# Optimization experiments

Hardware: AMD Instinct MI355X
Metric: run time of the kernel (lower is better)

## Reference

```python
import jax, jax.numpy as jnp
import numpy as np

ATOL = 1e-06
RTOL = 1e-06

def setup_inputs() -> dict:
    key = jax.random.key(0)
    ks = jax.random.split(key, 8)
    u = lambda k, shape: jax.random.uniform(k, shape, jnp.float32, -0.05, 0.05)
    return {
        "x": jax.random.normal(ks[0], (4096, 32, 32, 3), jnp.float32),
        "W_lstm": u(ks[1], (3, 16)),      # input kernel, gates [i,f,c,o]
        "U_lstm": u(ks[2], (4, 16)),      # recurrent kernel
        "dw_kernel": u(ks[3], (27, 27, 3, 5)),  # depthwise (kh,kw,in_c,mult)
        "pw_kernel": u(ks[4], (15, 4)),   # pointwise
        "conv_bias": u(ks[5], (4,)),
        "W_td": u(ks[6], (4096, 10)),
        "W_sc": u(ks[7], (4096, 10)),
    }

def _lstm_td(x, W, U):
    # TimeDistributed LSTM: x (B,32,32,3) -> treat axis1 as TD batch, axis2 as time
    B = x.shape[0]
    seq = x.reshape(B * 32, 32, 3)          # (N, T, F)
    xs = jnp.transpose(seq, (1, 0, 2))      # (T, N, F)
    N = seq.shape[0]
    h0 = jnp.zeros((N, 4), x.dtype)
    c0 = jnp.zeros((N, 4), x.dtype)

    def step(carry, xt):
        h, c = carry
        z = xt @ W + h @ U                  # (N, 16)
        zi, zf, zc, zo = jnp.split(z, 4, axis=-1)
        i = jax.nn.elu(zi)                  # recurrent_activation='elu'
        f = jax.nn.elu(zf)
        c = f * c + i * jax.nn.softmax(zc, axis=-1)  # activation='softmax'
        o = jax.nn.elu(zo)
        h = o * jax.nn.softmax(c, axis=-1)
        return (h, c), h

    _, hs = jax.lax.scan(step, (h0, c0), xs)        # (T, N, 4)
    return jnp.transpose(hs, (1, 0, 2)).reshape(B, 32, 32, 4)

def _sep_conv(x, dw_kernel, pw_kernel, conv_bias):
    # depthwise: Keras (kh,kw,C,M) -> lax HWIO grouped (kh,kw,1,C*M), channel-major order
    dw = dw_kernel.reshape(27, 27, 1, 15)
    y = jax.lax.conv_general_dilated(
        x, dw, window_strides=(1, 1), padding='SAME',
        feature_group_count=3,
        dimension_numbers=('NHWC', 'HWIO', 'NHWC'))   # (B,32,32,15)
    y = jnp.einsum('bhwc,cf->bhwf', y, pw_kernel) + conv_bias
    return jax.nn.sigmoid(y)                          # (B,32,32,4)

def reference(x, W_lstm, U_lstm, dw_kernel, pw_kernel, conv_bias, W_td, W_sc):
    B = x.shape[0]
    td = _lstm_td(x, W_lstm, U_lstm).reshape(B, -1) @ W_td   # (B,10)
    sc = _sep_conv(x, dw_kernel, pw_kernel, conv_bias).reshape(B, -1) @ W_sc
    diff = jnp.abs(td - sc)
    tol = ATOL + RTOL * jnp.abs(sc)
    return diff <= tol
```

## Files before the change

kernel.cpp:

```cpp
#include <hip/hip_runtime.h>
#include <math.h>

#define TD_OFF 0
#define WTDR_OFF 40960
#define SC_OFF 81920
#define BG_BYTE_OFF 524288

typedef __bf16 bf16x8 __attribute__((ext_vector_type(8)));
typedef float f32x16 __attribute__((ext_vector_type(16)));

union FragU { bf16x8 v; float4 f; };

__device__ __forceinline__ f32x16 mfma16(bf16x8 a, bf16x8 b, f32x16 c) {
    return __builtin_amdgcn_mfma_f32_32x32x16_bf16(a, b, c, 0, 0, 0);
}

__device__ __forceinline__ float eluf(float v) {
    return v > 0.f ? v : __expf(v) - 1.f;
}

__global__ __launch_bounds__(256) void prep(const float* __restrict__ dw,
                                            const float* __restrict__ pw,
                                            const float* __restrict__ Wtd,
                                            float* __restrict__ Wtdr,
                                            unsigned short* __restrict__ Bg) {
    int gid = blockIdx.x * 256 + threadIdx.x;
    if (gid < 40960) {
        int k = gid & 3;
        int r = gid >> 2;
        int row = r & 31; r >>= 5;
        int j = r % 10;
        int tt = r / 10;
        Wtdr[gid] = Wtd[(size_t)(row * 128 + tt * 4 + k) * 10 + j];
        return;
    }
    int g2 = gid - 40960;
    if (g2 >= 162 * 128) return;
    int n = g2 & 127;
    int s = g2 >> 7;
    int half = s & 1;
    int cd = s >> 1;
    int c = cd / 27, d = cd % 27;
    int w = n >> 2, f = n & 3;
    unsigned short* dsth = Bg + (size_t)s * 4096 + n * 16;
    unsigned short* dstl = dsth + 2048;
#pragma unroll
    for (int k = 0; k < 16; k++) {
        int xi = half * 16 + k;
        int dx = xi - w + 13;
        float v = 0.f;
        if (dx >= 0 && dx < 27) {
#pragma unroll
            for (int m = 0; m < 5; m++)
                v = fmaf(dw[((d * 27 + dx) * 3 + c) * 5 + m],
                         pw[(c * 5 + m) * 4 + f], v);
        }
        __bf16 h = (__bf16)v;
        __bf16 l = (__bf16)(v - (float)h);
        dsth[k] = __builtin_bit_cast(unsigned short, h);
        dstl[k] = __builtin_bit_cast(unsigned short, l);
    }
}

#define A_OFF 0
#define ZOFF 49152
#define SRED_OFF 49168
#define LDS_BYTES 49488

__global__ __launch_bounds__(256, 3) void fused(const float* __restrict__ x,
                                                const float* __restrict__ W,
                                                const float* __restrict__ U,
                                                const float* __restrict__ Wtdr,
                                                const unsigned short* __restrict__ Bg,
                                                const float* __restrict__ Wsc,
                                                const float* __restrict__ bias,
                                                float* __restrict__ td_out,
                                                float* __restrict__ sc_out) {
    __shared__ char LDS[LDS_BYTES] __attribute__((aligned(16)));
    int bx = blockIdx.x;
    int rem = bx % 3;
    int q = bx / 3;
    int t = threadIdx.x;

    if (rem == 2) {
        float rW[48], rU[64];
        const float4* W4 = (const float4*)W;
        const float4* U4 = (const float4*)U;
#pragma unroll
        for (int i = 0; i < 12; i++) {
            float4 qv = W4[i];
            rW[i * 4 + 0] = qv.x; rW[i * 4 + 1] = qv.y;
            rW[i * 4 + 2] = qv.z; rW[i * 4 + 3] = qv.w;
        }
#pragma unroll
        for (int i = 0; i < 16; i++) {
            float4 qv = U4[i];
            rU[i * 4 + 0] = qv.x; rU[i * 4 + 1] = qv.y;
            rU[i * 4 + 2] = qv.z; rU[i * 4 + 3] = qv.w;
        }

        int n = q * 256 + t;
        int row = n & 31;
        const float4* xp4 = (const float4*)(x + (size_t)n * 96);

        float h0 = 0, h1 = 0, h2 = 0, h3 = 0;
        float c0 = 0, c1 = 0, c2 = 0, c3 = 0;
        float acc[10];
#pragma unroll
        for (int j = 0; j < 10; j++) acc[j] = 0.f;

        for (int g = 0; g < 8; g++) {
            float4 q0 = xp4[g * 3 + 0], q1 = xp4[g * 3 + 1], q2 = xp4[g * 3 + 2];
            float xr[12] = {q0.x, q0.y, q0.z, q0.w, q1.x, q1.y,
                            q1.z, q1.w, q2.x, q2.y, q2.z, q2.w};
#pragma unroll
            for (int st = 0; st < 4; st++) {
                int tt = g * 4 + st;
                float x0 = xr[st * 3 + 0], x1 = xr[st * 3 + 1], x2 = xr[st * 3 + 2];
                float z[16];
#pragma unroll
                for (int k = 0; k < 16; k++)
                    z[k] = x0 * rW[k] + x1 * rW[16 + k] + x2 * rW[32 + k]
                         + h0 * rU[k] + h1 * rU[16 + k] + h2 * rU[32 + k] + h3 * rU[48 + k];

                float ig0 = eluf(z[0]),  ig1 = eluf(z[1]),  ig2 = eluf(z[2]),  ig3 = eluf(z[3]);
                float fg0 = eluf(z[4]),  fg1 = eluf(z[5]),  fg2 = eluf(z[6]),  fg3 = eluf(z[7]);
                float og0 = eluf(z[12]), og1 = eluf(z[13]), og2 = eluf(z[14]), og3 = eluf(z[15]);

                float zm = fmaxf(fmaxf(z[8], z[9]), fmaxf(z[10], z[11]));
                float e0 = __expf(z[8] - zm), e1 = __expf(z[9] - zm);
                float e2 = __expf(z[10] - zm), e3 = __expf(z[11] - zm);
                float inv = 1.f / (e0 + e1 + e2 + e3);
                c0 = fg0 * c0 + ig0 * (e0 * inv);
                c1 = fg1 * c1 + ig1 * (e1 * inv);
                c2 = fg2 * c2 + ig2 * (e2 * inv);
                c3 = fg3 * c3 + ig3 * (e3 * inv);

                float cm = fmaxf(fmaxf(c0, c1), fmaxf(c2, c3));
                float p0 = __expf(c0 - cm), p1 = __expf(c1 - cm);
                float p2 = __expf(c2 - cm), p3 = __expf(c3 - cm);
                float pinv = 1.f / (p0 + p1 + p2 + p3);
                h0 = og0 * (p0 * pinv); h1 = og1 * (p1 * pinv);
                h2 = og2 * (p2 * pinv); h3 = og3 * (p3 * pinv);

                const float4* wr4 = (const float4*)(Wtdr + (size_t)tt * 1280) + row;
#pragma unroll
                for (int j = 0; j < 10; j++) {
                    float4 qv = wr4[j * 32];
                    acc[j] += h0 * qv.x + h1 * qv.y + h2 * qv.z + h3 * qv.w;
                }
            }
        }

#pragma unroll
        for (int off = 16; off >= 1; off >>= 1) {
#pragma unroll
            for (int j = 0; j < 10; j++) acc[j] += __shfl_xor(acc[j], off, 64);
        }
        int lane = t & 63;
        if (lane == 0 || lane == 32) {
            int b = n >> 5;
#pragma unroll
            for (int j = 0; j < 10; j++) td_out[b * 10 + j] = acc[j];
        }
        return;
    }

    int ci = q * 2 + rem;
    int l = t & 63;
    int wv = t >> 6;
    int m = l & 31;
    int sub = l >> 5;
    int img0 = (wv >> 1) * 2;
    int ntbase = (wv & 1) * 2;

    const char* bbase = (const char*)Bg + (size_t)ntbase * 1024 + m * 32 + sub * 16;
    FragU bufA[4], bufB[4];
#define LOADB(sv, arr) { const char* p_ = bbase + (size_t)(sv) * 8192;       \
        arr[0].f = *(const float4*)(p_);                         \
        arr[1].f = *(const float4*)(p_ + 4096);                  \
        arr[2].f = *(const float4*)(p_ + 1024);                  \
        arr[3].f = *(const float4*)(p_ + 5120); }

    LOADB(0, bufA);
    LOADB(1, bufB);

    const float4* xb4 = (const float4*)(x + (size_t)ci * 12288);
#pragma unroll
    for (int it = 0; it < 12; it++) {
        int fi = it * 256 + t;
        float4 qv = xb4[fi];
        float vals[4] = {qv.x, qv.y, qv.z, qv.w};
#pragma unroll
        for (int e = 0; e < 4; e++) {
            int pel = fi * 4 + e;
            int im = pel / 3072;
            int p = pel - im * 3072;
            int c = p % 3;
            int hw = p / 3;
            int w = hw & 31;
            int h = hw >> 5;
            int rec = A_OFF + im * 12288
                      + ((c * 8) + (w >> 4) * 2 + ((w >> 3) & 1)) * 512
                      + h * 16 + (w & 7) * 2;
            float v = vals[e];
            __bf16 hb = (__bf16)v;
            __bf16 lb = (__bf16)(v - (float)hb);
            *(__bf16*)(LDS + rec) = hb;
            *(__bf16*)(LDS + rec + 2048) = lb;
        }
    }
    if (t < 4) *(float*)(LDS + ZOFF + t * 4) = 0.f;
    __syncthreads();

    f32x16 acc00 = {0,0,0,0,0,0,0,0,0,0,0,0,0,0,0,0};
    f32x16 acc01 = acc00, acc10 = acc00, acc11 = acc00;

    int c = 0, d = 0, half = 0;

#define CHUNK(USE, SNEXT) {                                                   \
    int rowIdx = m + d - 13;                                                  \
    bool valid = (unsigned)rowIdx < 32u;                                      \
    int a0 = A_OFF + img0 * 12288 + (c * 8 + half * 2 + sub) * 512 + rowIdx * 16; \
    int ah0o = valid ? a0 : ZOFF;                                             \
    int al0o = valid ? (a0 + 2048) : ZOFF;                                    \
    int ah1o = valid ? (a0 + 12288) : ZOFF;                                   \
    int al1o = valid ? (a0 + 14336) : ZOFF;                                   \
    FragU ah0, al0, ah1, al1;                                                 \
    ah0.f = *(const float4*)(LDS + ah0o);                                     \
    al0.f = *(const float4*)(LDS + al0o);                                     \
    ah1.f = *(const float4*)(LDS + ah1o);                                     \
    al1.f = *(const float4*)(LDS + al1o);                                     \
    acc00 = mfma16(ah0.v, USE[0].v, acc00);                                   \
    acc01 = mfma16(ah0.v, USE[2].v, acc01);                                   \
    acc10 = mfma16(ah1.v, USE[0].v, acc10);                                   \
    acc11 = mfma16(ah1.v, USE[2].v, acc11);                                   \
    acc00 = mfma16(ah0.v, USE[1].v, acc00);                                   \
    acc01 = mfma16(ah0.v, USE[3].v, acc01);                                   \
    acc10 = mfma16(ah1.v, USE[1].v, acc10);                                   \
    acc11 = mfma16(ah1.v, USE[3].v, acc11);                                   \
    acc00 = mfma16(al0.v, USE[0].v, acc00);                                   \
    acc01 = mfma16(al0.v, USE[2].v, acc01);                                   \
    acc10 = mfma16(al1.v, USE[0].v, acc10);                                   \
    acc11 = mfma16(al1.v, USE[2].v, acc11);                                   \
    LOADB(SNEXT, USE);                                                        \
    half ^= 1;                                                                \
    if (!half) { d++; if (d == 27) { d = 0; c++; } }                          \
}

    for (int g = 0; g < 81; g++) {
        CHUNK(bufA, 2 * g + 2);
        CHUNK(bufB, 2 * g + 3);
    }

    float b4[4];
#pragma unroll
    for (int i = 0; i < 4; i++) b4[i] = bias[i];

    float part[2][10];
#pragma unroll
    for (int i = 0; i < 2; i++)
#pragma unroll
        for (int j = 0; j < 10; j++) part[i][j] = 0.f;

    f32x16 accs[2][2] = {{acc00, acc01}, {acc10, acc11}};
#pragma unroll
    for (int i2 = 0; i2 < 2; i2++) {
#pragma unroll
        for (int j2 = 0; j2 < 2; j2++) {
            int ncol = (ntbase + j2) * 32 + m;
            int wcol = ncol >> 2;
            int f = ncol & 3;
            f32x16 a = accs[i2][j2];
#pragma unroll
            for (int r = 0; r < 16; r++) {
                int h = (r & 3) + 8 * (r >> 2) + 4 * sub;
                float v = a[r] + b4[f];
                float sg = 1.f / (1.f + expf(-v));
                const float* wr = Wsc + (size_t)((h * 32 + wcol) * 4 + f) * 10;
#pragma unroll
                for (int j = 0; j < 10; j++) part[i2][j] = fmaf(sg, wr[j], part[i2][j]);
            }
        }
    }

#pragma unroll
    for (int off = 32; off >= 1; off >>= 1) {
#pragma unroll
        for (int i2 = 0; i2 < 2; i2++)
#pragma unroll
            for (int j = 0; j < 10; j++) part[i2][j] += __shfl_xor(part[i2][j], off, 64);
    }
    if (l == 0) {
        float* red = (float*)(LDS + SRED_OFF);
#pragma unroll
        for (int i2 = 0; i2 < 2; i2++)
#pragma unroll
            for (int j = 0; j < 10; j++) red[(wv * 2 + i2) * 10 + j] = part[i2][j];
    }
    __syncthreads();
    if (t < 40) {
        int img = t / 10, j = t % 10;
        const float* red = (const float*)(LDS + SRED_OFF);
        int pair = img >> 1, i2 = img & 1;
        float sv = red[((pair * 2) * 2 + i2) * 10 + j]
                 + red[((pair * 2 + 1) * 2 + i2) * 10 + j];
        sc_out[(ci * 4 + img) * 10 + j] = sv;
    }
}

__global__ __launch_bounds__(256) void cmp_k(const float* __restrict__ td,
                                             const float* __restrict__ sc,
                                             float* __restrict__ out) {
    int i = blockIdx.x * 256 + threadIdx.x;
    if (i < 40960) {
        float a = td[i];
        float s = sc[i];
        float tol = 1e-6f + 1e-6f * fabsf(s);
        out[i] = (fabsf(a - s) <= tol) ? 1.0f : 0.0f;
    }
}

extern "C" void kernel_launch(void* const* d_in, const int* in_sizes, int n_in,
                              void* d_out, int out_size, void* d_ws, size_t ws_size,
                              hipStream_t stream) {
    const float* x    = (const float*)d_in[0];
    const float* W    = (const float*)d_in[1];
    const float* U    = (const float*)d_in[2];
    const float* dw   = (const float*)d_in[3];
    const float* pw   = (const float*)d_in[4];
    const float* bias = (const float*)d_in[5];
    const float* Wtd  = (const float*)d_in[6];
    const float* Wsc  = (const float*)d_in[7];

    float* ws     = (float*)d_ws;
    float* td_acc = ws + TD_OFF;
    float* Wtdr   = ws + WTDR_OFF;
    float* sc_acc = ws + SC_OFF;
    unsigned short* Bg = (unsigned short*)((char*)d_ws + BG_BYTE_OFF);

    prep<<<241, 256, 0, stream>>>(dw, pw, Wtd, Wtdr, Bg);
    fused<<<1536, 256, 0, stream>>>(x, W, U, Wtdr, Bg, Wsc, bias, td_acc, sc_acc);
    cmp_k<<<160, 256, 0, stream>>>(td_acc, sc_acc, (float*)d_out);
}
```

Before: 369.3 us.

## Remap conv waves to one N-tile across four images with triple-buffered B loads

Each wave now handles a single 32-column output tile for all four images instead of two tiles for two images. Each wave therefore loads half as much B-fragment data from global memory per chunk, and those loads go through a three-deep rotating buffer. The input staging is rewritten so each thread reads contiguous float4 rows and writes packed 16-byte bf16 hi/lo fragments to LDS instead of scalar 2-byte stores. The epilogue loads each Wsc row once and reuses it for all four images. In exchange, each chunk issues twice as many LDS A-fragment reads, and the larger partial arrays and extra buffer raise register pressure.

```diff
diff --git a/kernel.cpp b/kernel.cpp
--- a/kernel.cpp
+++ b/kernel.cpp
@@ -65,7 +65,7 @@
 #define A_OFF 0
 #define ZOFF 49152
 #define SRED_OFF 49168
-#define LDS_BYTES 49488
+#define LDS_BYTES 49808
 
 __global__ __launch_bounds__(256, 3) void fused(const float* __restrict__ x,
                                                 const float* __restrict__ W,
@@ -171,140 +171,141 @@
     int wv = t >> 6;
     int m = l & 31;
     int sub = l >> 5;
-    int img0 = (wv >> 1) * 2;
-    int ntbase = (wv & 1) * 2;
-
-    const char* bbase = (const char*)Bg + (size_t)ntbase * 1024 + m * 32 + sub * 16;
-    FragU bufA[4], bufB[4];
+
+    const char* bbase = (const char*)Bg + (size_t)wv * 1024 + m * 32 + sub * 16;
+    FragU bufA[2], bufB[2], bufC[2];
 #define LOADB(sv, arr) { const char* p_ = bbase + (size_t)(sv) * 8192;       \
-        arr[0].f = *(const float4*)(p_);                         \
-        arr[1].f = *(const float4*)(p_ + 4096);                  \
-        arr[2].f = *(const float4*)(p_ + 1024);                  \
-        arr[3].f = *(const float4*)(p_ + 5120); }
+        arr[0].f = *(const float4*)(p_);                             \
+        arr[1].f = *(const float4*)(p_ + 4096); }
 
     LOADB(0, bufA);
     LOADB(1, bufB);
-
-    const float4* xb4 = (const float4*)(x + (size_t)ci * 12288);
-#pragma unroll
-    for (int it = 0; it < 12; it++) {
-        int fi = it * 256 + t;
-        float4 qv = xb4[fi];
-        float vals[4] = {qv.x, qv.y, qv.z, qv.w};
-#pragma unroll
-        for (int e = 0; e < 4; e++) {
-            int pel = fi * 4 + e;
-            int im = pel / 3072;
-            int p = pel - im * 3072;
-            int c = p % 3;
-            int hw = p / 3;
-            int w = hw & 31;
-            int h = hw >> 5;
-            int rec = A_OFF + im * 12288
-                      + ((c * 8) + (w >> 4) * 2 + ((w >> 3) & 1)) * 512
-                      + h * 16 + (w & 7) * 2;
-            float v = vals[e];
-            __bf16 hb = (__bf16)v;
-            __bf16 lb = (__bf16)(v - (float)hb);
-            *(__bf16*)(LDS + rec) = hb;
-            *(__bf16*)(LDS + rec + 2048) = lb;
+    LOADB(2, bufC);
+
+    const float* xb = x + (size_t)ci * 12288;
+#pragma unroll
+    for (int rep = 0; rep < 2; rep++) {
+        int u = rep * 256 + t;
+        int im = u >> 7;
+        int woct = (u >> 5) & 3;
+        int h = u & 31;
+        const float4* src = (const float4*)(xb + im * 3072 + h * 96 + woct * 24);
+        float xr[24];
+#pragma unroll
+        for (int i = 0; i < 6; i++) {
+            float4 qv = src[i];
+            xr[i * 4 + 0] = qv.x; xr[i * 4 + 1] = qv.y;
+            xr[i * 4 + 2] = qv.z; xr[i * 4 + 3] = qv.w;
+        }
+#pragma unroll
+        for (int c = 0; c < 3; c++) {
+            FragU hiF, loF;
+#pragma unroll
+            for (int k = 0; k < 8; k++) {
+                float v = xr[k * 3 + c];
+                __bf16 hb = (__bf16)v;
+                hiF.v[k] = hb;
+                loF.v[k] = (__bf16)(v - (float)hb);
+            }
+            int rec = A_OFF + im * 12288 + (c * 8 + woct) * 512 + h * 16;
+            *(float4*)(LDS + rec) = hiF.f;
+            *(float4*)(LDS + rec + 2048) = loF.f;
         }
     }
     if (t < 4) *(float*)(LDS + ZOFF + t * 4) = 0.f;
     __syncthreads();
 
-    f32x16 acc00 = {0,0,0,0,0,0,0,0,0,0,0,0,0,0,0,0};
-    f32x16 acc01 = acc00, acc10 = acc00, acc11 = acc00;
+    f32x16 acc0 = {0,0,0,0,0,0,0,0,0,0,0,0,0,0,0,0};
+    f32x16 acc1 = acc0, acc2 = acc0, acc3 = acc0;
 
     int c = 0, d = 0, half = 0;
 
 #define CHUNK(USE, SNEXT) {                                                   \
     int rowIdx = m + d - 13;                                                  \
     bool valid = (unsigned)rowIdx < 32u;                                      \
-    int a0 = A_OFF + img0 * 12288 + (c * 8 + half * 2 + sub) * 512 + rowIdx * 16; \
-    int ah0o = valid ? a0 : ZOFF;                                             \
-    int al0o = valid ? (a0 + 2048) : ZOFF;                                    \
-    int ah1o = valid ? (a0 + 12288) : ZOFF;                                   \
-    int al1o = valid ? (a0 + 14336) : ZOFF;                                   \
-    FragU ah0, al0, ah1, al1;                                                 \
-    ah0.f = *(const float4*)(LDS + ah0o);                                     \
-    al0.f = *(const float4*)(LDS + al0o);                                     \
-    ah1.f = *(const float4*)(LDS + ah1o);                                     \
-    al1.f = *(const float4*)(LDS + al1o);                                     \
-    acc00 = mfma16(ah0.v, USE[0].v, acc00);                                   \
-    acc01 = mfma16(ah0.v, USE[2].v, acc01);                                   \
-    acc10 = mfma16(ah1.v, USE[0].v, acc10);                                   \
-    acc11 = mfma16(ah1.v, USE[2].v, acc11);                                   \
-    acc00 = mfma16(ah0.v, USE[1].v, acc00);                                   \
-    acc01 = mfma16(ah0.v, USE[3].v, acc01);                                   \
-    acc10 = mfma16(ah1.v, USE[1].v, acc10);                                   \
-    acc11 = mfma16(ah1.v, USE[3].v, acc11);                                   \
-    acc00 = mfma16(al0.v, USE[0].v, acc00);                                   \
-    acc01 = mfma16(al0.v, USE[2].v, acc01);                                   \
-    acc10 = mfma16(al1.v, USE[0].v, acc10);                                   \
-    acc11 = mfma16(al1.v, USE[2].v, acc11);                                   \
+    int a0 = A_OFF + (c * 8 + half * 2 + sub) * 512 + rowIdx * 16;            \
+    FragU ah0, ah1, ah2, ah3, al0, al1, al2, al3;                             \
+    ah0.f = *(const float4*)(LDS + (valid ? a0           : ZOFF));            \
+    ah1.f = *(const float4*)(LDS + (valid ? a0 + 12288   : ZOFF));            \
+    ah2.f = *(const float4*)(LDS + (valid ? a0 + 24576   : ZOFF));            \
+    ah3.f = *(const float4*)(LDS + (valid ? a0 + 36864   : ZOFF));            \
+    al0.f = *(const float4*)(LDS + (valid ? a0 + 2048    : ZOFF));            \
+    al1.f = *(const float4*)(LDS + (valid ? a0 + 14336   : ZOFF));            \
+    al2.f = *(const float4*)(LDS + (valid ? a0 + 26624   : ZOFF));            \
+    al3.f = *(const float4*)(LDS + (valid ? a0 + 38912   : ZOFF));            \
+    acc0 = mfma16(ah0.v, USE[0].v, acc0);                                     \
+    acc1 = mfma16(ah1.v, USE[0].v, acc1);                                     \
+    acc2 = mfma16(ah2.v, USE[0].v, acc2);                                     \
+    acc3 = mfma16(ah3.v, USE[0].v, acc3);                                     \
+    acc0 = mfma16(ah0.v, USE[1].v, acc0);                                     \
+    acc1 = mfma16(ah1.v, USE[1].v, acc1);                                     \
+    acc2 = mfma16(ah2.v, USE[1].v, acc2);                                     \
+    acc3 = mfma16(ah3.v, USE[1].v, acc3);                                     \
+    acc0 = mfma16(al0.v, USE[0].v, acc0);                                     \
+    acc1 = mfma16(al1.v, USE[0].v, acc1);                                     \
+    acc2 = mfma16(al2.v, USE[0].v, acc2);                                     \
+    acc3 = mfma16(al3.v, USE[0].v, acc3);                                     \
     LOADB(SNEXT, USE);                                                        \
     half ^= 1;                                                                \
     if (!half) { d++; if (d == 27) { d = 0; c++; } }                          \
 }
 
-    for (int g = 0; g < 81; g++) {
-        CHUNK(bufA, 2 * g + 2);
-        CHUNK(bufB, 2 * g + 3);
+    for (int g = 0; g < 54; g++) {
+        CHUNK(bufA, 3 * g + 3);
+        CHUNK(bufB, 3 * g + 4);
+        CHUNK(bufC, 3 * g + 5);
     }
 
     float b4[4];
 #pragma unroll
     for (int i = 0; i < 4; i++) b4[i] = bias[i];
 
-    float part[2][10];
-#pragma unroll
-    for (int i = 0; i < 2; i++)
+    float part[4][10];
+#pragma unroll
+    for (int i = 0; i < 4; i++)
 #pragma unroll
         for (int j = 0; j < 10; j++) part[i][j] = 0.f;
 
-    f32x16 accs[2][2] = {{acc00, acc01}, {acc10, acc11}};
-#pragma unroll
-    for (int i2 = 0; i2 < 2; i2++) {
-#pragma unroll
-        for (int j2 = 0; j2 < 2; j2++) {
-            int ncol = (ntbase + j2) * 32 + m;
-            int wcol = ncol >> 2;
-            int f = ncol & 3;
-            f32x16 a = accs[i2][j2];
-#pragma unroll
-            for (int r = 0; r < 16; r++) {
-                int h = (r & 3) + 8 * (r >> 2) + 4 * sub;
-                float v = a[r] + b4[f];
-                float sg = 1.f / (1.f + expf(-v));
-                const float* wr = Wsc + (size_t)((h * 32 + wcol) * 4 + f) * 10;
-#pragma unroll
-                for (int j = 0; j < 10; j++) part[i2][j] = fmaf(sg, wr[j], part[i2][j]);
-            }
+    f32x16 accs[4] = {acc0, acc1, acc2, acc3};
+    int ncol = wv * 32 + m;
+    int wcol = ncol >> 2;
+    int f = ncol & 3;
+#pragma unroll
+    for (int r = 0; r < 16; r++) {
+        int h = (r & 3) + 8 * (r >> 2) + 4 * sub;
+        const float* wr = Wsc + (size_t)((h * 32 + wcol) * 4 + f) * 10;
+        float wreg[10];
+#pragma unroll
+        for (int j = 0; j < 10; j++) wreg[j] = wr[j];
+#pragma unroll
+        for (int im = 0; im < 4; im++) {
+            float v = accs[im][r] + b4[f];
+            float sg = 1.f / (1.f + expf(-v));
+#pragma unroll
+            for (int j = 0; j < 10; j++) part[im][j] = fmaf(sg, wreg[j], part[im][j]);
         }
     }
 
 #pragma unroll
     for (int off = 32; off >= 1; off >>= 1) {
 #pragma unroll
-        for (int i2 = 0; i2 < 2; i2++)
-#pragma unroll
-            for (int j = 0; j < 10; j++) part[i2][j] += __shfl_xor(part[i2][j], off, 64);
+        for (int im = 0; im < 4; im++)
+#pragma unroll
+            for (int j = 0; j < 10; j++) part[im][j] += __shfl_xor(part[im][j], off, 64);
     }
     if (l == 0) {
         float* red = (float*)(LDS + SRED_OFF);
 #pragma unroll
-        for (int i2 = 0; i2 < 2; i2++)
-#pragma unroll
-            for (int j = 0; j < 10; j++) red[(wv * 2 + i2) * 10 + j] = part[i2][j];
+        for (int im = 0; im < 4; im++)
+#pragma unroll
+            for (int j = 0; j < 10; j++) red[(wv * 4 + im) * 10 + j] = part[im][j];
     }
     __syncthreads();
     if (t < 40) {
         int img = t / 10, j = t % 10;
         const float* red = (const float*)(LDS + SRED_OFF);
-        int pair = img >> 1, i2 = img & 1;
-        float sv = red[((pair * 2) * 2 + i2) * 10 + j]
-                 + red[((pair * 2 + 1) * 2 + i2) * 10 + j];
+        float sv = red[(0 * 4 + img) * 10 + j] + red[(1 * 4 + img) * 10 + j]
+                 + red[(2 * 4 + img) * 10 + j] + red[(3 * 4 + img) * 10 + j];
         sc_out[(ci * 4 + img) * 10 + j] = sv;
     }
 }
```

Measured after the change: 361.7 us. 2.1% less time.
